# Kernel optimization log

Hardware: AMD Instinct MI355X
Metric: run time of the kernel (lower is better)

## Reference

```python
import jax, jax.numpy as jnp
import numpy as np

LAGRANGE_ORDER = 5  # fixed, as in the torch module


def _lagrange_weights(alpha):
    """Vectorised Lagrange weights of length L+1. alpha: [B,N] -> [B,N,L+1]."""
    L = LAGRANGE_ORDER
    j = jnp.arange(L + 1, dtype=alpha.dtype)
    u = alpha[..., None] - j                          # [B,N,L+1]
    denom = j[:, None] - j[None, :]                   # [L+1,L+1]
    mask = ~jnp.eye(L + 1, dtype=bool)
    num = jnp.where(mask, u[..., None, :], jnp.ones_like(u)[..., None, :])
    den = jnp.where(mask, denom, jnp.ones_like(denom))
    return (num / den).prod(axis=-1)                  # [B,N,L+1]


def setup_inputs() -> dict:
    key = jax.random.key(0)
    k1, k2, k3 = jax.random.split(key, 3)
    B, N = 16, 16384
    # fractional period in samples, in [40, 100) -> max floor(f0)=99, K=99+5+3=107<=108
    f0 = 40.0 + 60.0 * jax.random.uniform(k1, (B, N), dtype=jnp.float32)
    x = jax.random.normal(k2, (B, N), dtype=jnp.float32)
    l_b = jax.random.uniform(k3, (B, N, 2), dtype=jnp.float32)  # (g, p) in [0,1]
    return {"f0": f0, "x": x, "l_b": l_b, "K": 108}


def reference(f0, x, l_b, K):
    B, N = x.shape
    L = LAGRANGE_ORDER
    # design_loop: (g, p) -> loop taps [b0, a1]; gain capped <1 for stability
    g = 0.99 * l_b[..., 0]
    p = l_b[..., 1]
    b0 = g * (1.0 - p)                                # [B,N]
    a1 = g * p
    # tune_f0: subtract low-frequency phase delay of (b0 + a1 z^-1)
    f0c = f0 - a1 / (b0 + a1 + 1e-7)
    # Lagrange centre & weights
    z = jnp.floor(f0c).astype(jnp.int32)
    z_center = z - L // 2                             # [B,N]
    alpha = f0c - z_center.astype(f0.dtype)
    w = _lagrange_weights(alpha)                      # [B,N,L+1]
    # compute_resonator_matrix: loop filter convolved with fractional delay -> block [B,N,L+2]
    block = (b0[..., None] * jnp.pad(w, ((0, 0), (0, 0), (0, 1)))
             + a1[..., None] * jnp.pad(w, ((0, 0), (0, 0), (1, 0))))
    # scatter (-block) into A; LPC lag k+1 lives in column k
    cols = z_center[..., None] - 1 + jnp.arange(L + 2)  # [B,N,L+2]
    cols = jnp.clip(cols, 0, K - 1)
    A = jnp.zeros((B, N, K), x.dtype).at[
        jnp.arange(B)[:, None, None], jnp.arange(N)[None, :, None], cols
    ].add(-block)
    # sample_wise_lpc: y[n] = x[n] - sum_k A[n,k] * y[n-1-k], zero init state
    def step(buf, inp):
        a_n, x_n = inp                                 # [B,K], [B]
        y_n = x_n - jnp.sum(a_n * buf, axis=-1)
        buf = jnp.concatenate([y_n[:, None], buf[:, :-1]], axis=1)
        return buf, y_n
    buf0 = jnp.zeros((B, K), x.dtype)
    _, ys = jax.lax.scan(step, buf0, (A.transpose(1, 0, 2), x.T))  # ys: [N,B]
    return ys.T
```

## Files before the change

### kernel.cpp

```cpp
#include <hip/hip_runtime.h>
#include <math.h>


#define B_    16
#define N_    16384
#define S_    16
#define NSEG  1024
#define NITER 28
#define RUNS  104
#define RG    26
#define CHUNK 37

#define CW_FLOATS (B_ * N_ * 8)
#define TG_FLOATS (B_ * S_ * RUNS * RUNS)
#define ST_FLOATS (B_ * S_ * RUNS)

__device__ __forceinline__ void diffks_coeffs(float f0v, float lbg, float lbp,
                                              int n, float4& lo, float4& hi) {
  float g  = 0.99f * lbg;
  float p  = lbp;
  float b0 = g * (1.0f - p);
  float a1 = g * p;
  float f0c = f0v - a1 / (b0 + a1 + 1e-7f);
  int   zc  = (int)floorf(f0c) - 2;
  float alpha = f0c - (float)zc;
  float u0 = alpha;
  float u1 = alpha - 1.0f;
  float u2 = alpha - 2.0f;
  float u3 = alpha - 3.0f;
  float u4 = alpha - 4.0f;
  float u5 = alpha - 5.0f;
  float w0 = u1 * u2 * u3 * u4 * u5 * (-1.0f / 120.0f);
  float w1 = u0 * u2 * u3 * u4 * u5 * ( 1.0f /  24.0f);
  float w2 = u0 * u1 * u3 * u4 * u5 * (-1.0f /  12.0f);
  float w3 = u0 * u1 * u2 * u4 * u5 * ( 1.0f /  12.0f);
  float w4 = u0 * u1 * u2 * u3 * u5 * (-1.0f /  24.0f);
  float w5 = u0 * u1 * u2 * u3 * u4 * ( 1.0f / 120.0f);
  lo.x = b0 * w0;
  lo.y = fmaf(b0, w1, a1 * w0);
  lo.z = fmaf(b0, w2, a1 * w1);
  lo.w = fmaf(b0, w3, a1 * w2);
  hi.x = fmaf(b0, w4, a1 * w3);
  hi.y = fmaf(b0, w5, a1 * w4);
  hi.z = a1 * w5;
  hi.w = __int_as_float((n - 6 - zc) & 255);
}

__global__ __launch_bounds__(1024) void diffks_phase1(
    const float* __restrict__ f0, const float* __restrict__ lb,
    const float* __restrict__ x, float* __restrict__ cw,
    float* __restrict__ Tg) {
  const int bs = blockIdx.x;
  const int b  = bs >> 4, s = bs & 15;
  const int n0 = s << 10;
  const int tid = threadIdx.x;

  __shared__ float4 hist4[256 * RG];
  __shared__ float4 stA[NSEG], stB[NSEG];
  __shared__ float  stX[NSEG];

  for (int i = tid; i < 256 * RG; i += 1024) hist4[i] = float4{0, 0, 0, 0};

  {
    const int n = n0 + tid;
    const size_t gi = (size_t)b * N_ + n;
    float4 lo, hi;
    diffks_coeffs(f0[gi], lb[2 * gi], lb[2 * gi + 1], n, lo, hi);
    stA[tid] = lo; stB[tid] = hi; stX[tid] = x[gi];
    float4* c4 = (float4*)cw;
    c4[2 * gi]     = lo;
    c4[2 * gi + 1] = hi;
  }
  __syncthreads();

  if (tid >= 1 && tid <= 103) {
    const int row = tid, r = 103 - tid;
    ((float*)&hist4[row * RG + (r >> 2)])[r & 3] = 1.0f;
  }
  __syncthreads();

  const int  l   = tid / RG;
  const int  rg  = tid - l * RG;
  const bool actT = (l < CHUNK);

  for (int t = 0; t < NITER; ++t) {
    const int prel = t * CHUNK + l;
    if (actT && prel < NSEG) {
      const float4 lo = stA[prel];
      const float4 hi = stB[prel];
      const int base1 = (__float_as_int(hi.w) + 104) & 255;
      float4 acc = {0.0f, 0.0f, 0.0f,
                    (rg == RG - 1) ? stX[prel] : 0.0f};
      const float cm0 = hi.z, cm1 = hi.y, cm2 = hi.x, cm3 = lo.w,
                  cm4 = lo.z, cm5 = lo.y, cm6 = lo.x;
      const float c[7] = {cm0, cm1, cm2, cm3, cm4, cm5, cm6};
#pragma unroll
      for (int m = 0; m < 7; ++m) {
        const int row = (base1 + m) & 255;
        const float4 v = hist4[row * RG + rg];
        acc.x = fmaf(c[m], v.x, acc.x);
        acc.y = fmaf(c[m], v.y, acc.y);
        acc.z = fmaf(c[m], v.z, acc.z);
        acc.w = fmaf(c[m], v.w, acc.w);
      }
      hist4[((prel + 104) & 255) * RG + rg] = acc;
    }
    __syncthreads();
  }

  float* T = Tg + (size_t)bs * RUNS * RUNS;
  for (int idx = tid; idx < RUNS * RUNS; idx += 1024) {
    const int r = idx / RUNS;
    const int j = idx - r * RUNS;
    const int row = (103 - j) & 255;
    T[idx] = ((float*)&hist4[row * RG + (r >> 2)])[r & 3];
  }
}

__global__ __launch_bounds__(128) void diffks_phase2(
    const float* __restrict__ Tg, float* __restrict__ states) {
  const int b = blockIdx.x;
  const int j = threadIdx.x;
  __shared__ float cur[RUNS];
  if (j < RUNS) cur[j] = 0.0f;
  __syncthreads();
  for (int s = 0; s < S_; ++s) {
    if (j < RUNS) states[((size_t)b * S_ + s) * RUNS + j] = cur[j];
    const float* __restrict__ T = Tg + ((size_t)b * S_ + s) * RUNS * RUNS;
    float acc = 0.0f;
    if (j < 103) {
      const float* __restrict__ Tj = T + j;
      float a0 = 0.0f, a1 = 0.0f, a2 = 0.0f, a3 = 0.0f;
      int k = 0;
      for (; k + 3 < 103; k += 4) {
        a0 = fmaf(Tj[(k + 0) * RUNS], cur[k + 0], a0);
        a1 = fmaf(Tj[(k + 1) * RUNS], cur[k + 1], a1);
        a2 = fmaf(Tj[(k + 2) * RUNS], cur[k + 2], a2);
        a3 = fmaf(Tj[(k + 3) * RUNS], cur[k + 3], a3);
      }
      for (; k < 103; ++k) a0 = fmaf(Tj[k * RUNS], cur[k], a0);
      acc = ((a0 + a1) + (a2 + a3)) + Tj[103 * RUNS];
    }
    __syncthreads();
    if (j < 103) cur[j] = acc;
    __syncthreads();
  }
}

__global__ __launch_bounds__(64) void diffks_phase3(
    const float* __restrict__ x, const float* __restrict__ cw,
    const float* __restrict__ states, float* __restrict__ y) {
  const int bs = blockIdx.x;
  const int b  = bs >> 4, s = bs & 15;
  const int n0 = s << 10;
  const int lane = threadIdx.x;

  __shared__ float  ring[512];
  __shared__ float4 sC[2 * NSEG];
  __shared__ float4 sX4[NSEG / 4];
  __shared__ float4 sY4[NSEG / 4];

#pragma unroll
  for (int i = 0; i < 8; ++i) ring[lane + 64 * i] = 0.0f;

  const float4* __restrict__ c4 = ((const float4*)cw) + (size_t)(b * N_ + n0) * 2;
  const float4* __restrict__ x4 = (const float4*)(x + (size_t)b * N_ + n0);
  {
    float4 tmp[16];
#pragma unroll
    for (int half = 0; half < 2; ++half) {
      const int base = half * 1024;
#pragma unroll
      for (int q = 0; q < 16; ++q) tmp[q] = c4[base + 64 * q + lane];
#pragma unroll
      for (int q = 0; q < 16; ++q) sC[base + 64 * q + lane] = tmp[q];
    }
#pragma unroll
    for (int q = 0; q < 4; ++q) tmp[q] = x4[64 * q + lane];
#pragma unroll
    for (int q = 0; q < 4; ++q) sX4[64 * q + lane] = tmp[q];
  }
  __builtin_amdgcn_wave_barrier();
  asm volatile("" ::: "memory");

  const float* __restrict__ st = states + (size_t)bs * RUNS;
  {
    const float v = st[lane];
    if (lane < 103) { ring[255 - lane] = v; ring[511 - lane] = v; }
    if (lane < 39) {
      const float v2 = st[lane + 64];
      ring[191 - lane] = v2; ring[447 - lane] = v2;
    }
  }
  __builtin_amdgcn_wave_barrier();
  asm volatile("" ::: "memory");

  const bool actL = (lane < CHUNK);
  for (int t = 0; t < NITER; ++t) {
    const int prel = t * CHUNK + lane;
    if (actL && prel < NSEG) {
      const float4 lo = sC[2 * prel];
      const float4 hi = sC[2 * prel + 1];
      const float  xv = ((const float*)sX4)[prel];
      const int base = __float_as_int(hi.w);
      const float r0 = ring[base + 0];
      const float r1 = ring[base + 1];
      const float r2 = ring[base + 2];
      const float r3 = ring[base + 3];
      const float r4 = ring[base + 4];
      const float r5 = ring[base + 5];
      const float r6 = ring[base + 6];
      const float s0 = fmaf(lo.x, r6, xv);
      const float s1 = fmaf(lo.y, r5, lo.z * r4);
      const float s2 = fmaf(lo.w, r3, hi.x * r2);
      const float s3 = fmaf(hi.y, r1, hi.z * r0);
      const float yv = (s0 + s1) + (s2 + s3);
      const int w = prel & 255;
      ring[w]       = yv;
      ring[w + 256] = yv;
      ((float*)sY4)[prel] = yv;
    }
    __builtin_amdgcn_wave_barrier();
    asm volatile("" ::: "memory");
  }

  float4* __restrict__ yb = (float4*)(y + (size_t)b * N_ + n0);
#pragma unroll
  for (int q = 0; q < 4; ++q) yb[64 * q + lane] = sY4[64 * q + lane];
}

__global__ __launch_bounds__(256) void diffks_coeff_fb(
    const float* __restrict__ f0, const float* __restrict__ lb,
    float* __restrict__ cw, int total, int Nmask) {
  int idx = blockIdx.x * blockDim.x + threadIdx.x;
  if (idx >= total) return;
  float4 lo, hi;
  diffks_coeffs(f0[idx], lb[2 * idx], lb[2 * idx + 1], idx & Nmask, lo, hi);
  float4* out4 = (float4*)cw;
  out4[2 * idx]     = lo;
  out4[2 * idx + 1] = hi;
}

__global__ __launch_bounds__(64) void diffks_scan_fb(
    const float* __restrict__ x, const float* __restrict__ cw,
    float* __restrict__ y, int N) {
  const int b    = blockIdx.x;
  const int lane = threadIdx.x;
  __shared__ float ring[512];
#pragma unroll
  for (int i = 0; i < 8; ++i) ring[lane + 64 * i] = 0.0f;
  __builtin_amdgcn_wave_barrier();
  asm volatile("" ::: "memory");
  const float4* __restrict__ c4 = (const float4*)(cw + (size_t)b * N * 8);
  const float*  __restrict__ xb = x + (size_t)b * N;
  float*        __restrict__ yb = y + (size_t)b * N;
  const bool act = (lane < CHUNK);
  const int nIter = (N + CHUNK - 1) / CHUNK;
  for (int t = 0; t < nIter; ++t) {
    const int n = t * CHUNK + lane;
    if (act && n < N) {
      const float4 lo = c4[2 * n];
      const float4 hi = c4[2 * n + 1];
      const float  xv = xb[n];
      const int base = __float_as_int(hi.w);
      const float r0 = ring[base + 0];
      const float r1 = ring[base + 1];
      const float r2 = ring[base + 2];
      const float r3 = ring[base + 3];
      const float r4 = ring[base + 4];
      const float r5 = ring[base + 5];
      const float r6 = ring[base + 6];
      const float s0 = fmaf(lo.x, r6, xv);
      const float s1 = fmaf(lo.y, r5, lo.z * r4);
      const float s2 = fmaf(lo.w, r3, hi.x * r2);
      const float s3 = fmaf(hi.y, r1, hi.z * r0);
      const float yv = (s0 + s1) + (s2 + s3);
      ring[n & 255]         = yv;
      ring[(n & 255) + 256] = yv;
      yb[n] = yv;
    }
    __builtin_amdgcn_wave_barrier();
    asm volatile("" ::: "memory");
  }
}

extern "C" void kernel_launch(void* const* d_in, const int* in_sizes, int n_in,
                              void* d_out, int out_size, void* d_ws, size_t ws_size,
                              hipStream_t stream) {
  const float* f0 = (const float*)d_in[0];
  const float* x  = (const float*)d_in[1];
  const float* lb = (const float*)d_in[2];
  float* out = (float*)d_out;

  const int total = in_sizes[0];
  float* cw = (float*)d_ws;
  const size_t need = (size_t)(CW_FLOATS + TG_FLOATS + ST_FLOATS) * 4;

  if (total == B_ * N_ && ws_size >= need) {
    float* Tg = cw + CW_FLOATS;
    float* st = Tg + TG_FLOATS;
    diffks_phase1<<<B_ * S_, 1024, 0, stream>>>(f0, lb, x, cw, Tg);
    diffks_phase2<<<B_, 128, 0, stream>>>(Tg, st);
    diffks_phase3<<<B_ * S_, 64, 0, stream>>>(x, cw, st, out);
  } else {
    const int N = total / B_;
    diffks_coeff_fb<<<(total + 255) / 256, 256, 0, stream>>>(f0, lb, cw, total, N - 1);
    diffks_scan_fb<<<B_, 64, 0, stream>>>(x, cw, out, N);
  }
}
```

Before: 119.6 us.

## Restructure three-phase scan: wave-local phase1 sweep, parallel phase2 matvec, recompute coeffs

Phase 1 now partitions the 104 history runs across 13 wavefronts, each stepping 32 samples per iteration with only wave barriers instead of block-wide syncs, using a padded row stride. Phase 2 splits the 104x104 transfer matvec across 8 thread groups with register-prefetched next matrix and a shared reduction. Phase 3 recomputes the filter coefficients from inputs instead of reading a coefficient workspace, which removes that global write and read. It also stores T transposed and carries the input term through an explicit constant-one state entry, so the data plumbing between phases changes.

```diff
diff --git a/kernel.cpp b/kernel.cpp
--- a/kernel.cpp
+++ b/kernel.cpp
@@ -8,8 +8,8 @@
 #define NSEG  1024
 #define NITER 28
 #define RUNS  104
-#define RG    26
 #define CHUNK 37
+#define RSTR  108
 
 #define CW_FLOATS (B_ * N_ * 8)
 #define TG_FLOATS (B_ * S_ * RUNS * RUNS)
@@ -46,187 +46,177 @@
   hi.w = __int_as_float((n - 6 - zc) & 255);
 }
 
-__global__ __launch_bounds__(1024) void diffks_phase1(
+__global__ __launch_bounds__(832) void diffks_phase1(
     const float* __restrict__ f0, const float* __restrict__ lb,
-    const float* __restrict__ x, float* __restrict__ cw,
-    float* __restrict__ Tg) {
+    const float* __restrict__ x, float* __restrict__ Tg) {
   const int bs = blockIdx.x;
   const int b  = bs >> 4, s = bs & 15;
   const int n0 = s << 10;
   const int tid = threadIdx.x;
 
-  __shared__ float4 hist4[256 * RG];
+  __shared__ __align__(16) float hist[256 * RSTR];
   __shared__ float4 stA[NSEG], stB[NSEG];
   __shared__ float  stX[NSEG];
 
-  for (int i = tid; i < 256 * RG; i += 1024) hist4[i] = float4{0, 0, 0, 0};
-
-  {
-    const int n = n0 + tid;
+  for (int i = tid; i < 256 * RSTR; i += 832) hist[i] = 0.0f;
+  for (int i = tid; i < NSEG; i += 832) {
+    const int n = n0 + i;
     const size_t gi = (size_t)b * N_ + n;
     float4 lo, hi;
     diffks_coeffs(f0[gi], lb[2 * gi], lb[2 * gi + 1], n, lo, hi);
-    stA[tid] = lo; stB[tid] = hi; stX[tid] = x[gi];
-    float4* c4 = (float4*)cw;
-    c4[2 * gi]     = lo;
-    c4[2 * gi + 1] = hi;
-  }
-  __syncthreads();
-
-  if (tid >= 1 && tid <= 103) {
-    const int row = tid, r = 103 - tid;
-    ((float*)&hist4[row * RG + (r >> 2)])[r & 3] = 1.0f;
-  }
-  __syncthreads();
-
-  const int  l   = tid / RG;
-  const int  rg  = tid - l * RG;
-  const bool actT = (l < CHUNK);
-
-  for (int t = 0; t < NITER; ++t) {
-    const int prel = t * CHUNK + l;
-    if (actT && prel < NSEG) {
-      const float4 lo = stA[prel];
-      const float4 hi = stB[prel];
-      const int base1 = (__float_as_int(hi.w) + 104) & 255;
-      float4 acc = {0.0f, 0.0f, 0.0f,
-                    (rg == RG - 1) ? stX[prel] : 0.0f};
-      const float cm0 = hi.z, cm1 = hi.y, cm2 = hi.x, cm3 = lo.w,
-                  cm4 = lo.z, cm5 = lo.y, cm6 = lo.x;
-      const float c[7] = {cm0, cm1, cm2, cm3, cm4, cm5, cm6};
-#pragma unroll
-      for (int m = 0; m < 7; ++m) {
-        const int row = (base1 + m) & 255;
-        const float4 v = hist4[row * RG + rg];
-        acc.x = fmaf(c[m], v.x, acc.x);
-        acc.y = fmaf(c[m], v.y, acc.y);
-        acc.z = fmaf(c[m], v.z, acc.z);
-        acc.w = fmaf(c[m], v.w, acc.w);
-      }
-      hist4[((prel + 104) & 255) * RG + rg] = acc;
-    }
+    stA[i] = lo; stB[i] = hi; stX[i] = x[gi];
+  }
+  __syncthreads();
+  if (tid < 103) hist[(103 - tid) * RSTR + tid] = 1.0f;
+  __syncthreads();
+
+  const int w  = tid >> 6;
+  const int ln = tid & 63;
+  const int l  = ln & 31;
+  const int h  = ln >> 5;
+  const int c0 = 8 * w + 4 * h;
+  const bool px = (w == 12) && (h == 1);
+
+  for (int t = 0; t < 32; ++t) {
+    const int p = 32 * t + l;
+    const float4 lo = stA[p];
+    const float4 hi = stB[p];
+    const int base1 = (__float_as_int(hi.w) + 104) & 255;
+    float4 acc;
+    acc.x = 0.0f; acc.y = 0.0f; acc.z = 0.0f;
+    acc.w = px ? stX[p] : 0.0f;
+    const float c[7] = {hi.z, hi.y, hi.x, lo.w, lo.z, lo.y, lo.x};
+#pragma unroll
+    for (int m = 0; m < 7; ++m) {
+      const int row = (base1 + m) & 255;
+      const float4 v = *(const float4*)&hist[row * RSTR + c0];
+      acc.x = fmaf(c[m], v.x, acc.x);
+      acc.y = fmaf(c[m], v.y, acc.y);
+      acc.z = fmaf(c[m], v.z, acc.z);
+      acc.w = fmaf(c[m], v.w, acc.w);
+    }
+    *(float4*)&hist[((p + 104) & 255) * RSTR + c0] = acc;
+    __builtin_amdgcn_wave_barrier();
+    asm volatile("" ::: "memory");
+  }
+  __syncthreads();
+
+  float* __restrict__ T = Tg + (size_t)bs * RUNS * RUNS;
+  for (int idx = tid; idx < RUNS * RUNS; idx += 832) {
+    const int j = idx / RUNS;
+    const int r = idx - j * RUNS;
+    T[idx] = (j < 103) ? hist[((103 - j) & 255) * RSTR + r] : 0.0f;
+  }
+}
+
+__global__ __launch_bounds__(832) void diffks_phase2(
+    const float* __restrict__ Tg, float* __restrict__ states) {
+  const int b   = blockIdx.x;
+  const int tid = threadIdx.x;
+  const int j   = tid % RUNS;
+  const int q   = tid / RUNS;
+  const int r0  = 13 * q;
+  __shared__ float cur[RUNS];
+  __shared__ float part[8][105];
+  if (tid < 103) cur[tid] = 0.0f;
+  if (tid == 103) cur[103] = 1.0f;
+  __syncthreads();
+
+  const float* __restrict__ Tb = Tg + (size_t)b * S_ * RUNS * RUNS;
+  float tv[13];
+#pragma unroll
+  for (int k = 0; k < 13; ++k)
+    tv[k] = (j < 103) ? Tb[(size_t)j * RUNS + r0 + k] : 0.0f;
+
+  for (int s = 0; s < S_; ++s) {
+    if (q == 0) states[((size_t)b * S_ + s) * RUNS + j] = cur[j];
+    float acc = 0.0f;
+#pragma unroll
+    for (int k = 0; k < 13; ++k) acc = fmaf(tv[k], cur[r0 + k], acc);
+    if (s + 1 < S_) {
+      const float* __restrict__ Tn = Tb + (size_t)(s + 1) * RUNS * RUNS;
+#pragma unroll
+      for (int k = 0; k < 13; ++k)
+        tv[k] = (j < 103) ? Tn[(size_t)j * RUNS + r0 + k] : 0.0f;
+    }
+    part[q][j] = acc;
     __syncthreads();
-  }
-
-  float* T = Tg + (size_t)bs * RUNS * RUNS;
-  for (int idx = tid; idx < RUNS * RUNS; idx += 1024) {
-    const int r = idx / RUNS;
-    const int j = idx - r * RUNS;
-    const int row = (103 - j) & 255;
-    T[idx] = ((float*)&hist4[row * RG + (r >> 2)])[r & 3];
-  }
-}
-
-__global__ __launch_bounds__(128) void diffks_phase2(
-    const float* __restrict__ Tg, float* __restrict__ states) {
-  const int b = blockIdx.x;
-  const int j = threadIdx.x;
-  __shared__ float cur[RUNS];
-  if (j < RUNS) cur[j] = 0.0f;
-  __syncthreads();
-  for (int s = 0; s < S_; ++s) {
-    if (j < RUNS) states[((size_t)b * S_ + s) * RUNS + j] = cur[j];
-    const float* __restrict__ T = Tg + ((size_t)b * S_ + s) * RUNS * RUNS;
-    float acc = 0.0f;
-    if (j < 103) {
-      const float* __restrict__ Tj = T + j;
-      float a0 = 0.0f, a1 = 0.0f, a2 = 0.0f, a3 = 0.0f;
-      int k = 0;
-      for (; k + 3 < 103; k += 4) {
-        a0 = fmaf(Tj[(k + 0) * RUNS], cur[k + 0], a0);
-        a1 = fmaf(Tj[(k + 1) * RUNS], cur[k + 1], a1);
-        a2 = fmaf(Tj[(k + 2) * RUNS], cur[k + 2], a2);
-        a3 = fmaf(Tj[(k + 3) * RUNS], cur[k + 3], a3);
-      }
-      for (; k < 103; ++k) a0 = fmaf(Tj[k * RUNS], cur[k], a0);
-      acc = ((a0 + a1) + (a2 + a3)) + Tj[103 * RUNS];
+    if (q == 0) {
+      float v = 0.0f;
+#pragma unroll
+      for (int qq = 0; qq < 8; ++qq) v += part[qq][j];
+      cur[j] = (j < 103) ? v : 1.0f;
     }
     __syncthreads();
-    if (j < 103) cur[j] = acc;
-    __syncthreads();
-  }
-}
-
-__global__ __launch_bounds__(64) void diffks_phase3(
-    const float* __restrict__ x, const float* __restrict__ cw,
-    const float* __restrict__ states, float* __restrict__ y) {
+  }
+}
+
+__global__ __launch_bounds__(256) void diffks_phase3(
+    const float* __restrict__ f0, const float* __restrict__ lb,
+    const float* __restrict__ x, const float* __restrict__ states,
+    float* __restrict__ y) {
   const int bs = blockIdx.x;
   const int b  = bs >> 4, s = bs & 15;
   const int n0 = s << 10;
-  const int lane = threadIdx.x;
-
-  __shared__ float  ring[512];
+  const int tid = threadIdx.x;
+
+  __shared__ __align__(16) float ring[512];
   __shared__ float4 sC[2 * NSEG];
-  __shared__ float4 sX4[NSEG / 4];
-  __shared__ float4 sY4[NSEG / 4];
-
-#pragma unroll
-  for (int i = 0; i < 8; ++i) ring[lane + 64 * i] = 0.0f;
-
-  const float4* __restrict__ c4 = ((const float4*)cw) + (size_t)(b * N_ + n0) * 2;
-  const float4* __restrict__ x4 = (const float4*)(x + (size_t)b * N_ + n0);
-  {
-    float4 tmp[16];
-#pragma unroll
-    for (int half = 0; half < 2; ++half) {
-      const int base = half * 1024;
-#pragma unroll
-      for (int q = 0; q < 16; ++q) tmp[q] = c4[base + 64 * q + lane];
-#pragma unroll
-      for (int q = 0; q < 16; ++q) sC[base + 64 * q + lane] = tmp[q];
-    }
-#pragma unroll
-    for (int q = 0; q < 4; ++q) tmp[q] = x4[64 * q + lane];
-#pragma unroll
-    for (int q = 0; q < 4; ++q) sX4[64 * q + lane] = tmp[q];
-  }
-  __builtin_amdgcn_wave_barrier();
-  asm volatile("" ::: "memory");
-
+  __shared__ float  sX[NSEG];
+  __shared__ float  sY[NSEG];
+
+  for (int i = tid; i < 512; i += 256) ring[i] = 0.0f;
+  for (int i = tid; i < NSEG; i += 256) {
+    const int n = n0 + i;
+    const size_t gi = (size_t)b * N_ + n;
+    float4 lo, hi;
+    diffks_coeffs(f0[gi], lb[2 * gi], lb[2 * gi + 1], n, lo, hi);
+    sC[2 * i] = lo; sC[2 * i + 1] = hi; sX[i] = x[gi];
+  }
+  __syncthreads();
   const float* __restrict__ st = states + (size_t)bs * RUNS;
-  {
-    const float v = st[lane];
-    if (lane < 103) { ring[255 - lane] = v; ring[511 - lane] = v; }
-    if (lane < 39) {
-      const float v2 = st[lane + 64];
-      ring[191 - lane] = v2; ring[447 - lane] = v2;
-    }
-  }
-  __builtin_amdgcn_wave_barrier();
-  asm volatile("" ::: "memory");
-
-  const bool actL = (lane < CHUNK);
-  for (int t = 0; t < NITER; ++t) {
-    const int prel = t * CHUNK + lane;
-    if (actL && prel < NSEG) {
-      const float4 lo = sC[2 * prel];
-      const float4 hi = sC[2 * prel + 1];
-      const float  xv = ((const float*)sX4)[prel];
-      const int base = __float_as_int(hi.w);
-      const float r0 = ring[base + 0];
-      const float r1 = ring[base + 1];
-      const float r2 = ring[base + 2];
-      const float r3 = ring[base + 3];
-      const float r4 = ring[base + 4];
-      const float r5 = ring[base + 5];
-      const float r6 = ring[base + 6];
-      const float s0 = fmaf(lo.x, r6, xv);
-      const float s1 = fmaf(lo.y, r5, lo.z * r4);
-      const float s2 = fmaf(lo.w, r3, hi.x * r2);
-      const float s3 = fmaf(hi.y, r1, hi.z * r0);
-      const float yv = (s0 + s1) + (s2 + s3);
-      const int w = prel & 255;
-      ring[w]       = yv;
-      ring[w + 256] = yv;
-      ((float*)sY4)[prel] = yv;
-    }
-    __builtin_amdgcn_wave_barrier();
-    asm volatile("" ::: "memory");
-  }
+  for (int k = tid; k < 103; k += 256) {
+    const float v = st[k];
+    ring[255 - k] = v;
+    ring[511 - k] = v;
+  }
+  __syncthreads();
+
+  if (tid < 64) {
+    const int lane = tid;
+    const bool act = (lane < CHUNK);
+    for (int t = 0; t < NITER; ++t) {
+      const int p = t * CHUNK + lane;
+      if (act && p < NSEG) {
+        const float4 lo = sC[2 * p];
+        const float4 hi = sC[2 * p + 1];
+        const float  xv = sX[p];
+        const int base = __float_as_int(hi.w);
+        const float r0 = ring[base + 0];
+        const float r1 = ring[base + 1];
+        const float r2 = ring[base + 2];
+        const float r3 = ring[base + 3];
+        const float r4 = ring[base + 4];
+        const float r5 = ring[base + 5];
+        const float r6 = ring[base + 6];
+        const float s0 = fmaf(lo.x, r6, xv);
+        const float s1 = fmaf(lo.y, r5, lo.z * r4);
+        const float s2 = fmaf(lo.w, r3, hi.x * r2);
+        const float s3 = fmaf(hi.y, r1, hi.z * r0);
+        const float yv = (s0 + s1) + (s2 + s3);
+        const int wsl = p & 255;
+        ring[wsl]       = yv;
+        ring[wsl + 256] = yv;
+        sY[p] = yv;
+      }
+      __builtin_amdgcn_wave_barrier();
+      asm volatile("" ::: "memory");
+    }
+  }
+  __syncthreads();
 
   float4* __restrict__ yb = (float4*)(y + (size_t)b * N_ + n0);
-#pragma unroll
-  for (int q = 0; q < 4; ++q) yb[64 * q + lane] = sY4[64 * q + lane];
+  yb[tid] = ((const float4*)sY)[tid];
 }
 
 __global__ __launch_bounds__(256) void diffks_coeff_fb(
@@ -293,17 +283,17 @@
   float* out = (float*)d_out;
 
   const int total = in_sizes[0];
-  float* cw = (float*)d_ws;
-  const size_t need = (size_t)(CW_FLOATS + TG_FLOATS + ST_FLOATS) * 4;
+  const size_t need = (size_t)(TG_FLOATS + ST_FLOATS) * 4;
 
   if (total == B_ * N_ && ws_size >= need) {
-    float* Tg = cw + CW_FLOATS;
+    float* Tg = (float*)d_ws;
     float* st = Tg + TG_FLOATS;
-    diffks_phase1<<<B_ * S_, 1024, 0, stream>>>(f0, lb, x, cw, Tg);
-    diffks_phase2<<<B_, 128, 0, stream>>>(Tg, st);
-    diffks_phase3<<<B_ * S_, 64, 0, stream>>>(x, cw, st, out);
+    diffks_phase1<<<B_ * S_, 832, 0, stream>>>(f0, lb, x, Tg);
+    diffks_phase2<<<B_, 832, 0, stream>>>(Tg, st);
+    diffks_phase3<<<B_ * S_, 256, 0, stream>>>(f0, lb, x, st, out);
   } else {
     const int N = total / B_;
+    float* cw = (float*)d_ws;
     diffks_coeff_fb<<<(total + 255) / 256, 256, 0, stream>>>(f0, lb, cw, total, N - 1);
     diffks_scan_fb<<<B_, 64, 0, stream>>>(x, cw, out, N);
   }
```

Result: slower. 185.1 us (+54.7%).
